# Performance work log

Measured on AMD Instinct MI355X. Metric: run time of the kernel, lower is better.

Reference implementation:

```python
import jax, jax.numpy as jnp
import numpy as np

B, S, D, H, F, E = 4, 1024, 1024, 16, 4096, 8
HD = D // H  # head dim


def setup_inputs() -> dict:
    key = jax.random.key(0)
    ks = jax.random.split(key, 8)
    p = lambda k, shp: jax.random.normal(k, shp, jnp.float32) * 0.02
    return {
        "x": jax.random.normal(ks[0], (B, S, D), jnp.float32),
        "mask": jnp.ones((B, S), jnp.int32),
        "in_proj_w": p(ks[1], (3 * D, D)),
        "in_proj_b": jnp.zeros((3 * D,), jnp.float32),
        "out_proj_w": p(ks[2], (D, D)),
        "out_proj_b": jnp.zeros((D,), jnp.float32),
        "ln1_g": jnp.ones((D,), jnp.float32),
        "ln1_b": jnp.zeros((D,), jnp.float32),
        "ln2_g": jnp.ones((D,), jnp.float32),
        "ln2_b": jnp.zeros((D,), jnp.float32),
        "gate_w": p(ks[3], (E, D)),
        "gate_b": jnp.zeros((E,), jnp.float32),
        "w1": p(ks[4], (E, F, D)),
        "b1": jnp.zeros((E, F), jnp.float32),
        "w2": p(ks[5], (E, D, F)),
        "b2": jnp.zeros((E, D), jnp.float32),
    }


def _layernorm(x, g, b, eps=1e-5):
    m = x.mean(-1, keepdims=True)
    v = ((x - m) ** 2).mean(-1, keepdims=True)
    return (x - m) / jnp.sqrt(v + eps) * g + b


def _mha(x, key_pad, in_proj_w, in_proj_b, out_proj_w, out_proj_b):
    # combined QKV projection as in torch nn.MultiheadAttention
    qkv = x @ in_proj_w.T + in_proj_b  # (B,S,3D)
    q, k, v = jnp.split(qkv, 3, axis=-1)
    def heads(t):
        return t.reshape(B, S, H, HD).transpose(0, 2, 1, 3)  # (B,H,S,HD)
    q, k, v = heads(q), heads(k), heads(v)
    scores = jnp.einsum("bhqd,bhkd->bhqk", q, k) / jnp.sqrt(jnp.float32(HD))
    scores = jnp.where(key_pad[:, None, None, :], -1e30, scores)
    attn = jax.nn.softmax(scores, axis=-1)
    out = jnp.einsum("bhqk,bhkd->bhqd", attn, v)  # (B,H,S,HD)
    out = out.transpose(0, 2, 1, 3).reshape(B, S, D)
    return out @ out_proj_w.T + out_proj_b


def _moe(x, gate_w, gate_b, w1, b1, w2, b2):
    logits = x @ gate_w.T + gate_b            # (B,S,E)
    probs = jax.nn.softmax(logits, axis=-1)
    # dense all-expert FFN (faithful to original: every expert computed)
    h = jax.nn.relu(jnp.einsum("bsd,efd->bsef", x, w1) + b1)   # (B,S,E,F)
    all_out = jnp.einsum("bsef,edf->bsed", h, w2) + b2          # (B,S,E,D)
    top_vals, top_idx = jax.lax.top_k(probs, 2)                 # (B,S,2)
    weights = top_vals / (top_vals.sum(-1, keepdims=True) + 1e-9)
    sel = jnp.take_along_axis(all_out, top_idx[..., None], axis=2)  # (B,S,2,D)
    return (sel * weights[..., None]).sum(axis=2)


def reference(x, mask, in_proj_w, in_proj_b, out_proj_w, out_proj_b,
              ln1_g, ln1_b, ln2_g, ln2_b, gate_w, gate_b, w1, b1, w2, b2):
    key_pad = mask == 0  # (B,S) bool
    attn_out = _mha(x, key_pad, in_proj_w, in_proj_b, out_proj_w, out_proj_b)
    x1 = _layernorm(x + attn_out, ln1_g, ln1_b)
    ff = _moe(x1, gate_w, gate_b, w1, b1, w2, b2)
    return _layernorm(x1 + ff, ln2_g, ln2_b)
```

## Files before the change

### kernel.cpp

```cpp
#include <hip/hip_runtime.h>

typedef __attribute__((ext_vector_type(8))) short bf16x8;
typedef __attribute__((ext_vector_type(4))) float f32x4;

#define DEV __device__ __forceinline__

static constexpr int Bb = 4, Sq = 1024, Dd = 1024, Hh = 16, HDd = 64, Ff = 4096, Ee = 8;
static constexpr int Nn = Bb * Sq;
static constexpr int TD = 3 * Dd;

DEV unsigned short f2bf(float x) {
  union { float f; unsigned u; } c; c.f = x;
  unsigned r = c.u + 0x7FFFu + ((c.u >> 16) & 1u);
  return (unsigned short)(r >> 16);
}

typedef const __attribute__((address_space(1))) unsigned int* gas_t;
typedef __attribute__((address_space(3))) unsigned int* las_t;
DEV void gload16(const void* g, void* l) {
  __builtin_amdgcn_global_load_lds((gas_t)g, (las_t)l, 16, 0, 0);
}

__global__ __launch_bounds__(256) void cvt_kernel(const float* __restrict__ in,
                                                  unsigned short* __restrict__ out) {
  int i = blockIdx.x * 256 + threadIdx.x;
  const float4 a = *(const float4*)(in + (size_t)i * 8);
  const float4 b = *(const float4*)(in + (size_t)i * 8 + 4);
  union { uint4 u; unsigned short s[8]; } pk;
  pk.s[0] = f2bf(a.x); pk.s[1] = f2bf(a.y); pk.s[2] = f2bf(a.z); pk.s[3] = f2bf(a.w);
  pk.s[4] = f2bf(b.x); pk.s[5] = f2bf(b.y); pk.s[6] = f2bf(b.z); pk.s[7] = f2bf(b.w);
  *(uint4*)(out + (size_t)i * 8) = pk.u;
}

template <int EPI>
__global__ __launch_bounds__(256) void gemm_bt(
    const unsigned short* __restrict__ A, const unsigned short* __restrict__ Bw,
    const float* __restrict__ bias, void* __restrict__ o0, void* __restrict__ o1,
    void* __restrict__ o2, int M, int Ncols, int K,
    const int* __restrict__ cnt, const int* __restrict__ off) {
  const int e = (EPI >= 2) ? blockIdx.z : 0;
  int mcnt = M;
  const unsigned short* Aptr = A;
  const unsigned short* Bptr = Bw;
  const float* biasptr = bias;
  int hbase = 0;
  if constexpr (EPI >= 2) {
    mcnt = cnt[e];
    Aptr = A + (size_t)off[e] * K;
    Bptr = Bw + (size_t)e * Ncols * K;
    biasptr = bias + e * Ncols;
    hbase = off[e];
  }
  int bx, by;
  {
    const int gx = gridDim.x, nwg = gx * gridDim.y;
    int orig = blockIdx.y * gx + blockIdx.x;
    int q = nwg >> 3, r = nwg & 7;
    int xcd = orig & 7, lin = orig >> 3;
    int wg = (xcd < r ? xcd * (q + 1) : r * (q + 1) + (xcd - r) * q) + lin;
    bx = wg % gx; by = wg / gx;
  }
  const int m0 = bx * 128;
  if (m0 >= mcnt) return;
  const int n0 = by * 128;

  __shared__ __align__(128) unsigned short As[128 * 32];
  __shared__ __align__(128) unsigned short Bs[128 * 32];

  const int tid = threadIdx.x;
  const int lane = tid & 63, wid = tid >> 6;
  const int wm = wid >> 1, wn = wid & 1;
  const int lr = lane & 15, lk = lane >> 4;

  const char* aSrc[2]; const char* bSrc[2];
  char* aDst[2]; char* bDst[2];
#pragma unroll
  for (int it = 0; it < 2; ++it) {
    int b = it * 4096 + tid * 16;
    int r = b >> 6;
    int colb = (b & 63) ^ (((r >> 1) & 3) << 4);
    int arow = (EPI >= 2) ? ((m0 + r < mcnt) ? (m0 + r) : 0) : (m0 + r);
    aSrc[it] = (const char*)(Aptr + (size_t)arow * K) + colb;
    bSrc[it] = (const char*)(Bptr + (size_t)(n0 + r) * K) + colb;
    aDst[it] = (char*)As + it * 4096 + wid * 1024;
    bDst[it] = (char*)Bs + it * 4096 + wid * 1024;
  }
  int aOff[4], bOff[4];
#pragma unroll
  for (int i = 0; i < 4; ++i) {
    int ra = wm * 64 + i * 16 + lr;
    aOff[i] = ra * 32 + ((lk ^ ((ra >> 1) & 3)) << 3);
    int rb = wn * 64 + i * 16 + lr;
    bOff[i] = rb * 32 + ((lk ^ ((rb >> 1) & 3)) << 3);
  }

  f32x4 acc[4][4] = {};

  for (int k0 = 0; k0 < K; k0 += 32) {
#pragma unroll
    for (int it = 0; it < 2; ++it) {
      gload16(aSrc[it] + (size_t)k0 * 2, aDst[it]);
      gload16(bSrc[it] + (size_t)k0 * 2, bDst[it]);
    }
    __syncthreads();
    bf16x8 af[4], bfv[4];
#pragma unroll
    for (int mi = 0; mi < 4; ++mi) af[mi] = *(const bf16x8*)&As[aOff[mi]];
#pragma unroll
    for (int ni = 0; ni < 4; ++ni) bfv[ni] = *(const bf16x8*)&Bs[bOff[ni]];
#pragma unroll
    for (int mi = 0; mi < 4; ++mi)
#pragma unroll
      for (int ni = 0; ni < 4; ++ni)
        acc[mi][ni] = __builtin_amdgcn_mfma_f32_16x16x32_bf16(af[mi], bfv[ni], acc[mi][ni], 0, 0, 0);
    __syncthreads();
  }

#pragma unroll
  for (int ni = 0; ni < 4; ++ni) {
    const int col = n0 + wn * 64 + ni * 16 + lr;
    const float bv = biasptr[col];
#pragma unroll
    for (int mi = 0; mi < 4; ++mi) {
#pragma unroll
      for (int i = 0; i < 4; ++i) {
        const int mloc = wm * 64 + mi * 16 + lk * 4 + i;
        float v = acc[mi][ni][i] + bv;
        if constexpr (EPI == 0) {
          int t = m0 + mloc;
          int which = col >> 10, jj = col & 1023, hh = jj >> 6, hd = jj & 63;
          int bb = t >> 10, s = t & 1023;
          unsigned short* dst = (which == 0) ? (unsigned short*)o0
                              : (which == 1) ? (unsigned short*)o1 : (unsigned short*)o2;
          dst[((size_t)(bb * Hh + hh) * Sq + s) * HDd + hd] = f2bf(v);
        } else if constexpr (EPI == 1) {
          ((float*)o0)[(size_t)(m0 + mloc) * Dd + col] = v;
        } else if constexpr (EPI == 2) {
          if (m0 + mloc < mcnt)
            ((unsigned short*)o0)[((size_t)hbase + m0 + mloc) * Ff + col] = f2bf(fmaxf(v, 0.f));
        } else {
          if (m0 + mloc < mcnt)
            ((float*)o0)[((size_t)hbase + m0 + mloc) * Dd + col] = v;
        }
      }
    }
  }
}

__global__ __launch_bounds__(256) void attn_kernel(
    const unsigned short* __restrict__ qb, const unsigned short* __restrict__ kb,
    const unsigned short* __restrict__ vb, const int* __restrict__ mask,
    unsigned short* __restrict__ attnb) {
  const int qt = blockIdx.x, h = blockIdx.y, b = blockIdx.z;
  const unsigned short* Q = qb + (size_t)(b * Hh + h) * Sq * HDd;
  const unsigned short* Kg = kb + (size_t)(b * Hh + h) * Sq * HDd;
  const unsigned short* Vg = vb + (size_t)(b * Hh + h) * Sq * HDd;

  __shared__ unsigned short Qs[64 * 72], Ks[64 * 72], Vt[64 * 72], Ps[64 * 72];
  __shared__ float Ssm[64 * 65];
  __shared__ float mS[64], lS[64], aS[64];
  __shared__ int mk[64];

  const int tid = threadIdx.x, lane = tid & 63, wid = tid >> 6;
  const int lr = lane & 15, lk = lane >> 4;

#pragma unroll
  for (int it = 0; it < 2; ++it) {
    int c = tid + it * 256; int r = c >> 3, kc = (c & 7) * 8;
    *(uint4*)&Qs[r * 72 + kc] = *(const uint4*)(Q + (size_t)(qt * 64 + r) * 64 + kc);
  }
  if (tid < 64) { mS[tid] = -1e30f; lS[tid] = 0.f; }

  f32x4 oacc[4] = {};

  for (int kt = 0; kt < 16; ++kt) {
    __syncthreads();
#pragma unroll
    for (int it = 0; it < 2; ++it) {
      int c = tid + it * 256; int r = c >> 3, kc = (c & 7) * 8;
      *(uint4*)&Ks[r * 72 + kc] = *(const uint4*)(Kg + (size_t)(kt * 64 + r) * 64 + kc);
    }
    {
      int kk = tid >> 2, hg = (tid & 3) * 16;
      union { uint4 u[2]; unsigned short s[16]; } tv;
      tv.u[0] = *(const uint4*)(Vg + (size_t)(kt * 64 + kk) * 64 + hg);
      tv.u[1] = *(const uint4*)(Vg + (size_t)(kt * 64 + kk) * 64 + hg + 8);
#pragma unroll
      for (int j = 0; j < 16; ++j) Vt[(hg + j) * 72 + kk] = tv.s[j];
    }
    if (tid < 64) mk[tid] = mask[b * Sq + kt * 64 + tid];
    __syncthreads();

    f32x4 sacc[4] = {};
#pragma unroll
    for (int ks = 0; ks < 2; ++ks) {
      bf16x8 aq = *(const bf16x8*)&Qs[(wid * 16 + lr) * 72 + ks * 32 + lk * 8];
#pragma unroll
      for (int ni = 0; ni < 4; ++ni) {
        bf16x8 bk = *(const bf16x8*)&Ks[(ni * 16 + lr) * 72 + ks * 32 + lk * 8];
        sacc[ni] = __builtin_amdgcn_mfma_f32_16x16x32_bf16(aq, bk, sacc[ni], 0, 0, 0);
      }
    }
#pragma unroll
    for (int ni = 0; ni < 4; ++ni)
#pragma unroll
      for (int i = 0; i < 4; ++i) {
        int r = wid * 16 + lk * 4 + i, cc = ni * 16 + lr;
        float v = sacc[ni][i] * 0.125f;
        if (mk[cc] == 0) v = -1e30f;
        Ssm[r * 65 + cc] = v;
      }
    __syncthreads();
    {
      int r = tid >> 2, cg = (tid & 3) * 16;
      float xv[16];
#pragma unroll
      for (int j = 0; j < 16; ++j) xv[j] = Ssm[r * 65 + cg + j];
      float mx = xv[0];
#pragma unroll
      for (int j = 1; j < 16; ++j) mx = fmaxf(mx, xv[j]);
      mx = fmaxf(mx, __shfl_xor(mx, 1));
      mx = fmaxf(mx, __shfl_xor(mx, 2));
      float mprev = mS[r];
      float mnew = fmaxf(mprev, mx);
      float sum = 0.f;
      union { uint4 u[2]; unsigned short s[16]; } pb;
#pragma unroll
      for (int j = 0; j < 16; ++j) {
        float pv = expf(xv[j] - mnew);
        sum += pv; pb.s[j] = f2bf(pv);
      }
      sum += __shfl_xor(sum, 1);
      sum += __shfl_xor(sum, 2);
      *(uint4*)&Ps[r * 72 + cg] = pb.u[0];
      *(uint4*)&Ps[r * 72 + cg + 8] = pb.u[1];
      if ((tid & 3) == 0) {
        float alpha = expf(mprev - mnew);
        mS[r] = mnew; aS[r] = alpha; lS[r] = lS[r] * alpha + sum;
      }
    }
    __syncthreads();
#pragma unroll
    for (int ni = 0; ni < 4; ++ni)
#pragma unroll
      for (int i = 0; i < 4; ++i)
        oacc[ni][i] *= aS[wid * 16 + lk * 4 + i];
#pragma unroll
    for (int ks = 0; ks < 2; ++ks) {
      bf16x8 ap = *(const bf16x8*)&Ps[(wid * 16 + lr) * 72 + ks * 32 + lk * 8];
#pragma unroll
      for (int ni = 0; ni < 4; ++ni) {
        bf16x8 bv = *(const bf16x8*)&Vt[(ni * 16 + lr) * 72 + ks * 32 + lk * 8];
        oacc[ni] = __builtin_amdgcn_mfma_f32_16x16x32_bf16(ap, bv, oacc[ni], 0, 0, 0);
      }
    }
  }
  __syncthreads();
#pragma unroll
  for (int ni = 0; ni < 4; ++ni)
#pragma unroll
    for (int i = 0; i < 4; ++i) {
      int r = wid * 16 + lk * 4 + i;
      int q = qt * 64 + r;
      float v = oacc[ni][i] / lS[r];
      attnb[((size_t)(b * Sq + q)) * Dd + h * 64 + ni * 16 + lr] = f2bf(v);
    }
}

__global__ __launch_bounds__(256) void ln_kernel(
    const float* __restrict__ a, const float* __restrict__ b2,
    const float* __restrict__ g, const float* __restrict__ beta,
    float* __restrict__ outf, unsigned short* __restrict__ outb) {
  const int t = blockIdx.x, tid = threadIdx.x;
  float4 v = *(const float4*)(a + (size_t)t * Dd + tid * 4);
  {
    float4 u = *(const float4*)(b2 + (size_t)t * Dd + tid * 4);
    v.x += u.x; v.y += u.y; v.z += u.z; v.w += u.w;
  }
  const int lane = tid & 63, wid = tid >> 6;
  float s = v.x + v.y + v.z + v.w;
  for (int sh = 1; sh < 64; sh <<= 1) s += __shfl_xor(s, sh);
  __shared__ float red[4], red2[4];
  if (lane == 0) red[wid] = s;
  __syncthreads();
  float mean = (red[0] + red[1] + red[2] + red[3]) * (1.f / Dd);
  float dx = v.x - mean, dy = v.y - mean, dz = v.z - mean, dw = v.w - mean;
  float q = dx * dx + dy * dy + dz * dz + dw * dw;
  for (int sh = 1; sh < 64; sh <<= 1) q += __shfl_xor(q, sh);
  if (lane == 0) red2[wid] = q;
  __syncthreads();
  float var = (red2[0] + red2[1] + red2[2] + red2[3]) * (1.f / Dd);
  float rstd = rsqrtf(var + 1e-5f);
  float4 gg = *(const float4*)(g + tid * 4);
  float4 bb = *(const float4*)(beta + tid * 4);
  float4 o;
  o.x = dx * rstd * gg.x + bb.x;
  o.y = dy * rstd * gg.y + bb.y;
  o.z = dz * rstd * gg.z + bb.z;
  o.w = dw * rstd * gg.w + bb.w;
  if (outf) *(float4*)(outf + (size_t)t * Dd + tid * 4) = o;
  if (outb) {
    ushort4 pk; pk.x = f2bf(o.x); pk.y = f2bf(o.y); pk.z = f2bf(o.z); pk.w = f2bf(o.w);
    *(ushort4*)(outb + (size_t)t * Dd + tid * 4) = pk;
  }
}

__global__ __launch_bounds__(256) void ln2_kernel(
    const float* __restrict__ x1f, const float* __restrict__ ffp,
    const int* __restrict__ inv, const float* __restrict__ wtok,
    const float* __restrict__ g, const float* __restrict__ beta,
    float* __restrict__ out) {
  const int t = blockIdx.x, tid = threadIdx.x;
  const int i0 = inv[2 * t], i1 = inv[2 * t + 1];
  const float w0 = wtok[2 * t], w1 = wtok[2 * t + 1];
  float4 v = *(const float4*)(x1f + (size_t)t * Dd + tid * 4);
  float4 u0 = *(const float4*)(ffp + (size_t)i0 * Dd + tid * 4);
  float4 u1 = *(const float4*)(ffp + (size_t)i1 * Dd + tid * 4);
  v.x += w0 * u0.x + w1 * u1.x; v.y += w0 * u0.y + w1 * u1.y;
  v.z += w0 * u0.z + w1 * u1.z; v.w += w0 * u0.w + w1 * u1.w;
  const int lane = tid & 63, wid = tid >> 6;
  float s = v.x + v.y + v.z + v.w;
  for (int sh = 1; sh < 64; sh <<= 1) s += __shfl_xor(s, sh);
  __shared__ float red[4], red2[4];
  if (lane == 0) red[wid] = s;
  __syncthreads();
  float mean = (red[0] + red[1] + red[2] + red[3]) * (1.f / Dd);
  float dx = v.x - mean, dy = v.y - mean, dz = v.z - mean, dw = v.w - mean;
  float q = dx * dx + dy * dy + dz * dz + dw * dw;
  for (int sh = 1; sh < 64; sh <<= 1) q += __shfl_xor(q, sh);
  if (lane == 0) red2[wid] = q;
  __syncthreads();
  float var = (red2[0] + red2[1] + red2[2] + red2[3]) * (1.f / Dd);
  float rstd = rsqrtf(var + 1e-5f);
  float4 gg = *(const float4*)(g + tid * 4);
  float4 bb = *(const float4*)(beta + tid * 4);
  float4 o;
  o.x = dx * rstd * gg.x + bb.x;
  o.y = dy * rstd * gg.y + bb.y;
  o.z = dz * rstd * gg.z + bb.z;
  o.w = dw * rstd * gg.w + bb.w;
  *(float4*)(out + (size_t)t * Dd + tid * 4) = o;
}

__global__ __launch_bounds__(256) void route_kernel(
    const float* __restrict__ x1f, const float* __restrict__ gw, const float* __restrict__ gb,
    int* __restrict__ cnt, int* __restrict__ tokslot, float* __restrict__ wtok) {
  __shared__ float gws[Ee * Dd];
  const int tid = threadIdx.x;
#pragma unroll
  for (int it = 0; it < 8; ++it) {
    int idx = (tid + it * 256) * 4;
    *(float4*)&gws[idx] = *(const float4*)(gw + idx);
  }
  __syncthreads();
  const int lane = tid & 63, wid = tid >> 6;
  for (int it = 0; it < 16; ++it) {
    int t = blockIdx.x * 64 + wid * 16 + it;
    float acc[Ee] = {};
    for (int i = 0; i < 16; ++i) {
      float xv = x1f[(size_t)t * Dd + i * 64 + lane];
#pragma unroll
      for (int e = 0; e < Ee; ++e) acc[e] += xv * gws[e * Dd + i * 64 + lane];
    }
#pragma unroll
    for (int e = 0; e < Ee; ++e) {
      float vv = acc[e];
      for (int sh = 1; sh < 64; sh <<= 1) vv += __shfl_xor(vv, sh);
      acc[e] = vv;
    }
    if (lane == 0) {
      float lg[Ee];
#pragma unroll
      for (int e = 0; e < Ee; ++e) lg[e] = acc[e] + gb[e];
      float m = lg[0];
#pragma unroll
      for (int e = 1; e < Ee; ++e) m = fmaxf(m, lg[e]);
      float p[Ee], ssum = 0.f;
#pragma unroll
      for (int e = 0; e < Ee; ++e) { p[e] = expf(lg[e] - m); ssum += p[e]; }
      int e0 = 0;
#pragma unroll
      for (int e = 1; e < Ee; ++e) if (p[e] > p[e0]) e0 = e;
      int e1 = -1;
#pragma unroll
      for (int e = 0; e < Ee; ++e) {
        if (e == e0) continue;
        if (e1 < 0 || p[e] > p[e1]) e1 = e;
      }
      float v0 = p[e0] / ssum, v1 = p[e1] / ssum;
      float wsum = v0 + v1 + 1e-9f;
      wtok[t * 2] = v0 / wsum; wtok[t * 2 + 1] = v1 / wsum;
      int p0 = atomicAdd(&cnt[e0], 1);
      tokslot[e0 * Nn + p0] = t * 2;
      int p1 = atomicAdd(&cnt[e1], 1);
      tokslot[e1 * Nn + p1] = t * 2 + 1;
    }
  }
}

__global__ void offsets_kernel(const int* __restrict__ cnt, int* __restrict__ off) {
  if (threadIdx.x == 0) {
    int s = 0;
    for (int e = 0; e < Ee; ++e) { off[e] = s; s += cnt[e]; }
    off[Ee] = s;
  }
}

__global__ __launch_bounds__(256) void pack_kernel(
    const unsigned short* __restrict__ x1b, const int* __restrict__ tokslot,
    const int* __restrict__ off, unsigned short* __restrict__ xg,
    int* __restrict__ inv) {
  const int tid = threadIdx.x;
  const int g = blockIdx.x * 8 + (tid >> 5);
  const int l = tid & 31;
  int e = 0;
#pragma unroll
  for (int k = 1; k < Ee; ++k) if (g >= off[k]) e = k;
  const int ent = tokslot[e * Nn + (g - off[e])];
  const int trow = ent >> 1;
  if (l == 0) inv[ent] = g;
  const uint4* src = (const uint4*)(x1b + (size_t)trow * Dd);
  uint4* dst = (uint4*)(xg + (size_t)g * Dd);
#pragma unroll
  for (int j = 0; j < 4; ++j) dst[l + j * 32] = src[l + j * 32];
}

extern "C" void kernel_launch(void* const* d_in, const int* in_sizes, int n_in,
                              void* d_out, int out_size, void* d_ws, size_t ws_size,
                              hipStream_t stream) {
  const float* x   = (const float*)d_in[0];
  const int*   msk = (const int*)d_in[1];
  const float* ipw = (const float*)d_in[2];
  const float* ipb = (const float*)d_in[3];
  const float* opw = (const float*)d_in[4];
  const float* opb = (const float*)d_in[5];
  const float* g1  = (const float*)d_in[6];
  const float* be1 = (const float*)d_in[7];
  const float* g2  = (const float*)d_in[8];
  const float* be2 = (const float*)d_in[9];
  const float* gw  = (const float*)d_in[10];
  const float* gb  = (const float*)d_in[11];
  const float* w1  = (const float*)d_in[12];
  const float* b1  = (const float*)d_in[13];
  const float* w2  = (const float*)d_in[14];
  const float* b2  = (const float*)d_in[15];
  float* out = (float*)d_out;

  char* p = (char*)d_ws;
  auto carve = [&](size_t bytes) { char* r = p; p += (bytes + 255) & ~(size_t)255; return r; };
  unsigned short* xb   = (unsigned short*)carve((size_t)Nn * Dd * 2);
  unsigned short* qb   = (unsigned short*)carve((size_t)Nn * Dd * 2);
  unsigned short* kb   = (unsigned short*)carve((size_t)Nn * Dd * 2);
  unsigned short* vb   = (unsigned short*)carve((size_t)Nn * Dd * 2);
  float* proj          = (float*)carve((size_t)Nn * Dd * 4);
  float* x1f           = (float*)carve((size_t)Nn * Dd * 4);
  unsigned short* x1b  = (unsigned short*)carve((size_t)Nn * Dd * 2);
  unsigned short* xg   = (unsigned short*)carve((size_t)2 * Nn * Dd * 2);
  float* ffp           = (float*)carve((size_t)2 * Nn * Dd * 4);
  unsigned short* hbuf = (unsigned short*)carve((size_t)2 * Nn * Ff * 2);
  unsigned short* wbuf = (unsigned short*)carve((size_t)Ee * Ff * Dd * 2);
  int* cnt             = (int*)carve(64);
  int* off             = (int*)carve(64);
  int* tokslot         = (int*)carve((size_t)Ee * Nn * 4);
  float* wtok          = (float*)carve((size_t)2 * Nn * 4);
  int* inv             = (int*)carve((size_t)2 * Nn * 4);
  unsigned short* attnb = xb;

  cvt_kernel<<<Nn * Dd / 2048, 256, 0, stream>>>(x, xb);
  cvt_kernel<<<TD * Dd / 2048, 256, 0, stream>>>(ipw, wbuf);
  gemm_bt<0><<<dim3(Nn / 128, TD / 128), 256, 0, stream>>>(
      xb, wbuf, ipb, qb, kb, vb, Nn, TD, Dd, nullptr, nullptr);
  attn_kernel<<<dim3(Sq / 64, Hh, Bb), 256, 0, stream>>>(qb, kb, vb, msk, attnb);
  cvt_kernel<<<Dd * Dd / 2048, 256, 0, stream>>>(opw, wbuf);
  gemm_bt<1><<<dim3(Nn / 128, Dd / 128), 256, 0, stream>>>(
      attnb, wbuf, opb, proj, nullptr, nullptr, Nn, Dd, Dd, nullptr, nullptr);
  ln_kernel<<<Nn, 256, 0, stream>>>(x, proj, g1, be1, x1f, x1b);
  hipMemsetAsync(cnt, 0, 64, stream);
  route_kernel<<<Nn / 64, 256, 0, stream>>>(x1f, gw, gb, cnt, tokslot, wtok);
  offsets_kernel<<<1, 64, 0, stream>>>(cnt, off);
  pack_kernel<<<2 * Nn / 8, 256, 0, stream>>>(x1b, tokslot, off, xg, inv);
  cvt_kernel<<<Ee * Ff * Dd / 2048, 256, 0, stream>>>(w1, wbuf);
  gemm_bt<2><<<dim3(Nn / 128, Ff / 128, Ee), 256, 0, stream>>>(
      xg, wbuf, b1, hbuf, nullptr, nullptr, Nn, Ff, Dd, cnt, off);
  cvt_kernel<<<Ee * Dd * Ff / 2048, 256, 0, stream>>>(w2, wbuf);
  gemm_bt<3><<<dim3(Nn / 128, Dd / 128, Ee), 256, 0, stream>>>(
      hbuf, wbuf, b2, ffp, nullptr, nullptr, Nn, Dd, Ff, cnt, off);
  ln2_kernel<<<Nn, 256, 0, stream>>>(x1f, ffp, inv, wtok, g2, be2, out);
}
```

Before: 675.3 us.

## Pad expert groups to 128 rows and double GEMM K-tile to 64

Expert segments are padded to multiples of 128 rows, so the grouped MoE GEMMs launch a compact 2D grid over the padded total instead of an 8-deep z grid where most blocks exit early. Each tile now maps to exactly one expert, which removes per-row bounds checks and row clamping. The GEMM K step also goes from 32 to 64, which halves the number of barriers per K and doubles LDS use. Padding rows are zero-filled in pack, adding a little wasted compute for partial tiles.

```diff
diff --git a/kernel.cpp b/kernel.cpp
--- a/kernel.cpp
+++ b/kernel.cpp
@@ -8,6 +8,7 @@
 static constexpr int Bb = 4, Sq = 1024, Dd = 1024, Hh = 16, HDd = 64, Ff = 4096, Ee = 8;
 static constexpr int Nn = Bb * Sq;
 static constexpr int TD = 3 * Dd;
+static constexpr int PMAX = 2 * Nn + Ee * 128;
 
 DEV unsigned short f2bf(float x) {
   union { float f; unsigned u; } c; c.f = x;
@@ -37,20 +38,7 @@
     const unsigned short* __restrict__ A, const unsigned short* __restrict__ Bw,
     const float* __restrict__ bias, void* __restrict__ o0, void* __restrict__ o1,
     void* __restrict__ o2, int M, int Ncols, int K,
-    const int* __restrict__ cnt, const int* __restrict__ off) {
-  const int e = (EPI >= 2) ? blockIdx.z : 0;
-  int mcnt = M;
-  const unsigned short* Aptr = A;
-  const unsigned short* Bptr = Bw;
-  const float* biasptr = bias;
-  int hbase = 0;
-  if constexpr (EPI >= 2) {
-    mcnt = cnt[e];
-    Aptr = A + (size_t)off[e] * K;
-    Bptr = Bw + (size_t)e * Ncols * K;
-    biasptr = bias + e * Ncols;
-    hbase = off[e];
-  }
+    const int* __restrict__ poff) {
   int bx, by;
   {
     const int gx = gridDim.x, nwg = gx * gridDim.y;
@@ -61,58 +49,70 @@
     bx = wg % gx; by = wg / gx;
   }
   const int m0 = bx * 128;
-  if (m0 >= mcnt) return;
+  int e = 0;
+  if constexpr (EPI >= 2) {
+    if (m0 >= poff[Ee]) return;
+#pragma unroll
+    for (int k = 1; k < Ee; ++k) if (m0 >= poff[k]) e = k;
+  } else {
+    if (m0 >= M) return;
+  }
   const int n0 = by * 128;
-
-  __shared__ __align__(128) unsigned short As[128 * 32];
-  __shared__ __align__(128) unsigned short Bs[128 * 32];
+  const unsigned short* Bptr = Bw + (size_t)e * Ncols * K;
+  const float* biasptr = bias + e * Ncols;
+
+  __shared__ __align__(128) unsigned short As[128 * 64];
+  __shared__ __align__(128) unsigned short Bs[128 * 64];
 
   const int tid = threadIdx.x;
   const int lane = tid & 63, wid = tid >> 6;
   const int wm = wid >> 1, wn = wid & 1;
   const int lr = lane & 15, lk = lane >> 4;
 
-  const char* aSrc[2]; const char* bSrc[2];
-  char* aDst[2]; char* bDst[2];
-#pragma unroll
-  for (int it = 0; it < 2; ++it) {
+  const char* aSrc[4]; const char* bSrc[4];
+  char* aDst[4]; char* bDst[4];
+#pragma unroll
+  for (int it = 0; it < 4; ++it) {
     int b = it * 4096 + tid * 16;
-    int r = b >> 6;
-    int colb = (b & 63) ^ (((r >> 1) & 3) << 4);
-    int arow = (EPI >= 2) ? ((m0 + r < mcnt) ? (m0 + r) : 0) : (m0 + r);
-    aSrc[it] = (const char*)(Aptr + (size_t)arow * K) + colb;
+    int r = b >> 7;
+    int colb = (b & 127) ^ (((r >> 1) & 3) << 4);
+    aSrc[it] = (const char*)(A + (size_t)(m0 + r) * K) + colb;
     bSrc[it] = (const char*)(Bptr + (size_t)(n0 + r) * K) + colb;
     aDst[it] = (char*)As + it * 4096 + wid * 1024;
     bDst[it] = (char*)Bs + it * 4096 + wid * 1024;
   }
-  int aOff[4], bOff[4];
-#pragma unroll
-  for (int i = 0; i < 4; ++i) {
-    int ra = wm * 64 + i * 16 + lr;
-    aOff[i] = ra * 32 + ((lk ^ ((ra >> 1) & 3)) << 3);
-    int rb = wn * 64 + i * 16 + lr;
-    bOff[i] = rb * 32 + ((lk ^ ((rb >> 1) & 3)) << 3);
-  }
+  int aOff[2][4], bOff[2][4];
+#pragma unroll
+  for (int ks = 0; ks < 2; ++ks)
+#pragma unroll
+    for (int i = 0; i < 4; ++i) {
+      int ra = wm * 64 + i * 16 + lr;
+      aOff[ks][i] = ra * 64 + ks * 32 + ((lk ^ ((ra >> 1) & 3)) << 3);
+      int rb = wn * 64 + i * 16 + lr;
+      bOff[ks][i] = rb * 64 + ks * 32 + ((lk ^ ((rb >> 1) & 3)) << 3);
+    }
 
   f32x4 acc[4][4] = {};
 
-  for (int k0 = 0; k0 < K; k0 += 32) {
-#pragma unroll
-    for (int it = 0; it < 2; ++it) {
-      gload16(aSrc[it] + (size_t)k0 * 2, aDst[it]);
-      gload16(bSrc[it] + (size_t)k0 * 2, bDst[it]);
-    }
-    __syncthreads();
-    bf16x8 af[4], bfv[4];
-#pragma unroll
-    for (int mi = 0; mi < 4; ++mi) af[mi] = *(const bf16x8*)&As[aOff[mi]];
-#pragma unroll
-    for (int ni = 0; ni < 4; ++ni) bfv[ni] = *(const bf16x8*)&Bs[bOff[ni]];
-#pragma unroll
-    for (int mi = 0; mi < 4; ++mi)
-#pragma unroll
-      for (int ni = 0; ni < 4; ++ni)
-        acc[mi][ni] = __builtin_amdgcn_mfma_f32_16x16x32_bf16(af[mi], bfv[ni], acc[mi][ni], 0, 0, 0);
+  for (int k0 = 0; k0 < K; k0 += 64) {
+#pragma unroll
+    for (int it = 0; it < 4; ++it) gload16(aSrc[it] + (size_t)k0 * 2, aDst[it]);
+#pragma unroll
+    for (int it = 0; it < 4; ++it) gload16(bSrc[it] + (size_t)k0 * 2, bDst[it]);
+    __syncthreads();
+#pragma unroll
+    for (int ks = 0; ks < 2; ++ks) {
+      bf16x8 af[4], bfv[4];
+#pragma unroll
+      for (int mi = 0; mi < 4; ++mi) af[mi] = *(const bf16x8*)&As[aOff[ks][mi]];
+#pragma unroll
+      for (int ni = 0; ni < 4; ++ni) bfv[ni] = *(const bf16x8*)&Bs[bOff[ks][ni]];
+#pragma unroll
+      for (int mi = 0; mi < 4; ++mi)
+#pragma unroll
+        for (int ni = 0; ni < 4; ++ni)
+          acc[mi][ni] = __builtin_amdgcn_mfma_f32_16x16x32_bf16(af[mi], bfv[ni], acc[mi][ni], 0, 0, 0);
+    }
     __syncthreads();
   }
 
@@ -136,11 +136,9 @@
         } else if constexpr (EPI == 1) {
           ((float*)o0)[(size_t)(m0 + mloc) * Dd + col] = v;
         } else if constexpr (EPI == 2) {
-          if (m0 + mloc < mcnt)
-            ((unsigned short*)o0)[((size_t)hbase + m0 + mloc) * Ff + col] = f2bf(fmaxf(v, 0.f));
+          ((unsigned short*)o0)[(size_t)(m0 + mloc) * Ff + col] = f2bf(fmaxf(v, 0.f));
         } else {
-          if (m0 + mloc < mcnt)
-            ((float*)o0)[((size_t)hbase + m0 + mloc) * Dd + col] = v;
+          ((float*)o0)[(size_t)(m0 + mloc) * Dd + col] = v;
         }
       }
     }
@@ -398,31 +396,38 @@
   }
 }
 
-__global__ void offsets_kernel(const int* __restrict__ cnt, int* __restrict__ off) {
+__global__ void offsets_kernel(const int* __restrict__ cnt, int* __restrict__ poff) {
   if (threadIdx.x == 0) {
     int s = 0;
-    for (int e = 0; e < Ee; ++e) { off[e] = s; s += cnt[e]; }
-    off[Ee] = s;
+    for (int e = 0; e < Ee; ++e) { poff[e] = s; s += (cnt[e] + 127) & ~127; }
+    poff[Ee] = s;
   }
 }
 
 __global__ __launch_bounds__(256) void pack_kernel(
     const unsigned short* __restrict__ x1b, const int* __restrict__ tokslot,
-    const int* __restrict__ off, unsigned short* __restrict__ xg,
-    int* __restrict__ inv) {
+    const int* __restrict__ cnt, const int* __restrict__ poff,
+    unsigned short* __restrict__ xg, int* __restrict__ inv) {
   const int tid = threadIdx.x;
   const int g = blockIdx.x * 8 + (tid >> 5);
   const int l = tid & 31;
+  if (g >= poff[Ee]) return;
   int e = 0;
 #pragma unroll
-  for (int k = 1; k < Ee; ++k) if (g >= off[k]) e = k;
-  const int ent = tokslot[e * Nn + (g - off[e])];
-  const int trow = ent >> 1;
-  if (l == 0) inv[ent] = g;
-  const uint4* src = (const uint4*)(x1b + (size_t)trow * Dd);
+  for (int k = 1; k < Ee; ++k) if (g >= poff[k]) e = k;
+  const int pos = g - poff[e];
   uint4* dst = (uint4*)(xg + (size_t)g * Dd);
-#pragma unroll
-  for (int j = 0; j < 4; ++j) dst[l + j * 32] = src[l + j * 32];
+  if (pos < cnt[e]) {
+    const int ent = tokslot[e * Nn + pos];
+    if (l == 0) inv[ent] = g;
+    const uint4* src = (const uint4*)(x1b + (size_t)(ent >> 1) * Dd);
+#pragma unroll
+    for (int j = 0; j < 4; ++j) dst[l + j * 32] = src[l + j * 32];
+  } else {
+    const uint4 z = make_uint4(0, 0, 0, 0);
+#pragma unroll
+    for (int j = 0; j < 4; ++j) dst[l + j * 32] = z;
+  }
 }
 
 extern "C" void kernel_launch(void* const* d_in, const int* in_sizes, int n_in,
@@ -455,12 +460,12 @@
   float* proj          = (float*)carve((size_t)Nn * Dd * 4);
   float* x1f           = (float*)carve((size_t)Nn * Dd * 4);
   unsigned short* x1b  = (unsigned short*)carve((size_t)Nn * Dd * 2);
-  unsigned short* xg   = (unsigned short*)carve((size_t)2 * Nn * Dd * 2);
-  float* ffp           = (float*)carve((size_t)2 * Nn * Dd * 4);
-  unsigned short* hbuf = (unsigned short*)carve((size_t)2 * Nn * Ff * 2);
+  unsigned short* xg   = (unsigned short*)carve((size_t)PMAX * Dd * 2);
+  float* ffp           = (float*)carve((size_t)PMAX * Dd * 4);
+  unsigned short* hbuf = (unsigned short*)carve((size_t)PMAX * Ff * 2);
   unsigned short* wbuf = (unsigned short*)carve((size_t)Ee * Ff * Dd * 2);
   int* cnt             = (int*)carve(64);
-  int* off             = (int*)carve(64);
+  int* poff            = (int*)carve(64);
   int* tokslot         = (int*)carve((size_t)Ee * Nn * 4);
   float* wtok          = (float*)carve((size_t)2 * Nn * 4);
   int* inv             = (int*)carve((size_t)2 * Nn * 4);
@@ -469,21 +474,21 @@
   cvt_kernel<<<Nn * Dd / 2048, 256, 0, stream>>>(x, xb);
   cvt_kernel<<<TD * Dd / 2048, 256, 0, stream>>>(ipw, wbuf);
   gemm_bt<0><<<dim3(Nn / 128, TD / 128), 256, 0, stream>>>(
-      xb, wbuf, ipb, qb, kb, vb, Nn, TD, Dd, nullptr, nullptr);
+      xb, wbuf, ipb, qb, kb, vb, Nn, TD, Dd, nullptr);
   attn_kernel<<<dim3(Sq / 64, Hh, Bb), 256, 0, stream>>>(qb, kb, vb, msk, attnb);
   cvt_kernel<<<Dd * Dd / 2048, 256, 0, stream>>>(opw, wbuf);
   gemm_bt<1><<<dim3(Nn / 128, Dd / 128), 256, 0, stream>>>(
-      attnb, wbuf, opb, proj, nullptr, nullptr, Nn, Dd, Dd, nullptr, nullptr);
+      attnb, wbuf, opb, proj, nullptr, nullptr, Nn, Dd, Dd, nullptr);
   ln_kernel<<<Nn, 256, 0, stream>>>(x, proj, g1, be1, x1f, x1b);
   hipMemsetAsync(cnt, 0, 64, stream);
   route_kernel<<<Nn / 64, 256, 0, stream>>>(x1f, gw, gb, cnt, tokslot, wtok);
-  offsets_kernel<<<1, 64, 0, stream>>>(cnt, off);
-  pack_kernel<<<2 * Nn / 8, 256, 0, stream>>>(x1b, tokslot, off, xg, inv);
+  offsets_kernel<<<1, 64, 0, stream>>>(cnt, poff);
+  pack_kernel<<<PMAX / 8, 256, 0, stream>>>(x1b, tokslot, cnt, poff, xg, inv);
   cvt_kernel<<<Ee * Ff * Dd / 2048, 256, 0, stream>>>(w1, wbuf);
-  gemm_bt<2><<<dim3(Nn / 128, Ff / 128, Ee), 256, 0, stream>>>(
-      xg, wbuf, b1, hbuf, nullptr, nullptr, Nn, Ff, Dd, cnt, off);
+  gemm_bt<2><<<dim3(PMAX / 128, Ff / 128), 256, 0, stream>>>(
+      xg, wbuf, b1, hbuf, nullptr, nullptr, PMAX, Ff, Dd, poff);
   cvt_kernel<<<Ee * Dd * Ff / 2048, 256, 0, stream>>>(w2, wbuf);
-  gemm_bt<3><<<dim3(Nn / 128, Dd / 128, Ee), 256, 0, stream>>>(
-      hbuf, wbuf, b2, ffp, nullptr, nullptr, Nn, Dd, Ff, cnt, off);
+  gemm_bt<3><<<dim3(PMAX / 128, Dd / 128), 256, 0, stream>>>(
+      hbuf, wbuf, b2, ffp, nullptr, nullptr, PMAX, Dd, Ff, poff);
   ln2_kernel<<<Nn, 256, 0, stream>>>(x1f, ffp, inv, wtok, g2, be2, out);
 }
```

New measurement: 674.8 us. No clear change (-0.1%).
